# Optimization experiments

Measured on AMD Instinct MI355X. Metric: run time of the kernel, lower is better.

The kernel has to match this reference:

```python
import jax, jax.numpy as jnp
import numpy as np

B, FD, HD, G, WR = 256, 1024, 256, 64, 10.0  # batch, feature_dim, hidden_dim, grid_size, workspace_range


def _w(key, shape):
    return jax.random.normal(key, shape, dtype=jnp.float32) * 0.02


def setup_inputs() -> dict:
    key = jax.random.key(0)
    ks = jax.random.split(key, 16)
    # egocentric coordinate grid, indexing='ij', flattened to [G*G, 2]
    x = jnp.linspace(-WR / 2, WR / 2, G)
    xx, yy = jnp.meshgrid(x, x, indexing='ij')
    coords = jnp.stack([xx, yy], axis=-1).reshape(-1, 2).astype(jnp.float32)
    return {
        'features': jax.random.normal(ks[0], (B, FD), dtype=jnp.float32),
        'coords': coords,
        # context_encoder: 1024 -> 256 -> 128 -> 64
        'ce_w1': _w(ks[1], (FD, HD)), 'ce_b1': jnp.zeros((HD,), jnp.float32),
        'ce_w2': _w(ks[2], (HD, HD // 2)), 'ce_b2': jnp.zeros((HD // 2,), jnp.float32),
        'ce_w3': _w(ks[3], (HD // 2, 64)), 'ce_b3': jnp.zeros((64,), jnp.float32),
        # success_field_mlp: 66 -> 256 -> 256 -> 128 -> 1
        'sf_w1': _w(ks[4], (2 + 64, HD)), 'sf_b1': jnp.zeros((HD,), jnp.float32),
        'sf_w2': _w(ks[5], (HD, HD)), 'sf_b2': jnp.zeros((HD,), jnp.float32),
        'sf_w3': _w(ks[6], (HD, HD // 2)), 'sf_b3': jnp.zeros((HD // 2,), jnp.float32),
        'sf_w4': _w(ks[7], (HD // 2, 1)), 'sf_b4': jnp.zeros((1,), jnp.float32),
    }


def reference(features, coords, ce_w1, ce_b1, ce_w2, ce_b2, ce_w3, ce_b3,
              sf_w1, sf_b1, sf_w2, sf_b2, sf_w3, sf_b3, sf_w4, sf_b4):
    # context encoder: [B, 1024] -> [B, 64]
    z = jax.nn.relu(features @ ce_w1 + ce_b1)
    z = jax.nn.relu(z @ ce_w2 + ce_b2)
    z_c = z @ ce_w3 + ce_b3  # [B, 64]
    # first field layer split: concat([coords, z_c]) @ sf_w1 == coords@W[:2] + z_c@W[2:]
    cpart = coords @ sf_w1[:2]      # [G*G, HD]
    zpart = z_c @ sf_w1[2:]         # [B, HD]
    h = jax.nn.relu(cpart[None, :, :] + zpart[:, None, :] + sf_b1)  # [B, G*G, HD]
    h = jax.nn.relu(h @ sf_w2 + sf_b2)
    h = jax.nn.relu(h @ sf_w3 + sf_b3)
    logits = h @ sf_w4 + sf_b4      # [B, G*G, 1]
    success_fields = jax.nn.sigmoid(logits).reshape(features.shape[0], G, G)
    return success_fields
```

## Files before the change

kernel.cpp:

```cpp
#include <hip/hip_runtime.h>
#include <hip/hip_bf16.h>

typedef __bf16 bf16_t;
typedef __attribute__((ext_vector_type(4))) float f32x4;
typedef __attribute__((ext_vector_type(8))) int i32x8;

#define FD 1024
#define HD 256
#define GG 4096
#define HSTR 272

__device__ inline unsigned int pack4_fp8(float a, float b, float c, float d) {
    int v = __builtin_amdgcn_cvt_pk_fp8_f32(a, b, 0, false);
    v = __builtin_amdgcn_cvt_pk_fp8_f32(c, d, v, true);
    return (unsigned int)v;
}

#define MFMA_MX(A, B, C) \
    __builtin_amdgcn_mfma_scale_f32_16x16x128_f8f6f4((A), (B), (C), 0, 0, 0, 127, 0, 127)

__global__ __launch_bounds__(256) void prep_kernel(
    const float* __restrict__ ce_w1,
    const float* __restrict__ sf_w2,
    const float* __restrict__ sf_w3,
    float* __restrict__ w1t,
    unsigned int* __restrict__ w2t8,
    unsigned int* __restrict__ w3t8)
{
    int id = blockIdx.x * 256 + threadIdx.x;
    if (w1t != nullptr) {
        int j = id >> 10, k = id & 1023;
        w1t[id] = ce_w1[k * 256 + j];
    }
    if (id < 16384) {
        int n = id >> 6, k4 = (id & 63) << 2;
        w2t8[id] = pack4_fp8(sf_w2[(k4 + 0) * 256 + n], sf_w2[(k4 + 1) * 256 + n],
                             sf_w2[(k4 + 2) * 256 + n], sf_w2[(k4 + 3) * 256 + n]);
    }
    if (id < 8192) {
        int n = id >> 6, k4 = (id & 63) << 2;
        w3t8[id] = pack4_fp8(sf_w3[(k4 + 0) * 128 + n], sf_w3[(k4 + 1) * 128 + n],
                             sf_w3[(k4 + 2) * 128 + n], sf_w3[(k4 + 3) * 128 + n]);
    }
}

__global__ __launch_bounds__(256) void ce_kernel(
    const float* __restrict__ features,
    const float* __restrict__ ce_w1,
    const float* __restrict__ w1t,
    const float* __restrict__ ce_b1,
    const float* __restrict__ ce_w2, const float* __restrict__ ce_b2,
    const float* __restrict__ ce_w3, const float* __restrict__ ce_b3,
    const float* __restrict__ sf_w1,
    const float* __restrict__ sf_b1,
    float* __restrict__ zpart)
{
    __shared__ float fs[FD];
    __shared__ float z1[HD];
    __shared__ float z2[HD / 2];
    __shared__ float zc[64];
    const int b = blockIdx.x, t = threadIdx.x;

    #pragma unroll
    for (int i = 0; i < 4; ++i) fs[t + i * 256] = features[b * FD + t + i * 256];
    __syncthreads();

    {
        float s = ce_b1[t];
        if (w1t != nullptr) {
            const float4* wr = reinterpret_cast<const float4*>(w1t + t * FD);
            #pragma unroll 4
            for (int k = 0; k < FD / 4; ++k) {
                float4 w = wr[k];
                const float4 f = *reinterpret_cast<const float4*>(&fs[k * 4]);
                s = fmaf(w.x, f.x, s);
                s = fmaf(w.y, f.y, s);
                s = fmaf(w.z, f.z, s);
                s = fmaf(w.w, f.w, s);
            }
        } else {
            #pragma unroll 8
            for (int k = 0; k < FD; ++k) s = fmaf(fs[k], ce_w1[k * 256 + t], s);
        }
        z1[t] = s > 0.f ? s : 0.f;
    }
    __syncthreads();

    if (t < 128) {
        float s = ce_b2[t];
        #pragma unroll 8
        for (int k = 0; k < 256; ++k) s = fmaf(z1[k], ce_w2[k * 128 + t], s);
        z2[t] = s > 0.f ? s : 0.f;
    }
    __syncthreads();

    if (t < 64) {
        float s = ce_b3[t];
        #pragma unroll 8
        for (int k = 0; k < 128; ++k) s = fmaf(z2[k], ce_w3[k * 64 + t], s);
        zc[t] = s;
    }
    __syncthreads();

    {
        float s = sf_b1[t];
        #pragma unroll 8
        for (int k = 0; k < 64; ++k) s = fmaf(zc[k], sf_w1[(2 + k) * 256 + t], s);
        zpart[b * HD + t] = s;
    }
}

__global__ __launch_bounds__(512, 2) void field_kernel(
    const float* __restrict__ coords,
    const float* __restrict__ sf_w1,
    const float* __restrict__ zpart,
    const unsigned char* __restrict__ w2t8,
    const float* __restrict__ sf_b2,
    const unsigned char* __restrict__ w3t8,
    const float* __restrict__ sf_b3,
    const float* __restrict__ sf_w4,
    const float* __restrict__ sf_b4,
    float* __restrict__ out)
{
    __shared__ __attribute__((aligned(128))) unsigned char h1[4][64 * HSTR];
    __shared__ __attribute__((aligned(128))) unsigned char h2[4][64 * HSTR];
    __shared__ float partials[4][64][20];

    const int b = blockIdx.x;
    const int tid = threadIdx.x;
    const int wid = tid >> 6;
    const int lane = tid & 63;
    const int l15 = lane & 15;
    const int l4 = lane >> 4;
    const int koff = l4 * 32;

    const int cg1 = wid & 3;
    const int rg1 = wid >> 2;
    i32x8 b1f[2][4];
    #pragma unroll
    for (int ks = 0; ks < 2; ++ks)
        #pragma unroll
        for (int n = 0; n < 4; ++n)
            b1f[ks][n] = *reinterpret_cast<const i32x8*>(
                &w2t8[(cg1 * 64 + n * 16 + l15) * 256 + ks * 128 + koff]);

    const int cgrp = wid & 3, rhalf = wid >> 2;
    i32x8 w3f[2][2];
    #pragma unroll
    for (int ks = 0; ks < 2; ++ks)
        #pragma unroll
        for (int cb = 0; cb < 2; ++cb)
            w3f[ks][cb] = *reinterpret_cast<const i32x8*>(
                &w3t8[(cgrp * 32 + cb * 16 + l15) * 256 + ks * 128 + koff]);

    f32x4 b2r[4];
    #pragma unroll
    for (int n = 0; n < 4; ++n)
        b2r[n] = *reinterpret_cast<const f32x4*>(&sf_b2[cg1 * 64 + n * 16 + l4 * 4]);
    f32x4 b3r[2], w4r[2];
    #pragma unroll
    for (int cb = 0; cb < 2; ++cb) {
        b3r[cb] = *reinterpret_cast<const f32x4*>(&sf_b3[cgrp * 32 + cb * 16 + l4 * 4]);
        w4r[cb] = *reinterpret_cast<const f32x4*>(&sf_w4[cgrp * 32 + cb * 16 + l4 * 4]);
    }
    const float b4v = sf_b4[0];

    const int kc = tid & 31;
    const int rbase = tid >> 5;
    float zpf[8], waf[8], wbf[8];
    #pragma unroll
    for (int j = 0; j < 8; ++j) {
        zpf[j] = zpart[b * HD + kc * 8 + j];
        waf[j] = sf_w1[kc * 8 + j];
        wbf[j] = sf_w1[HD + kc * 8 + j];
    }
    float xvr[4];
    #pragma unroll
    for (int it = 0; it < 4; ++it)
        xvr[it] = coords[2 * (it * 16 + rbase) + 1];

    auto ld32 = [&](const unsigned char* p) -> i32x8 {
        uint4 a = *reinterpret_cast<const uint4*>(p);
        uint4 c = *reinterpret_cast<const uint4*>(p + 16);
        i32x8 r;
        r[0] = a.x; r[1] = a.y; r[2] = a.z; r[3] = a.w;
        r[4] = c.x; r[5] = c.y; r[6] = c.z; r[7] = c.w;
        return r;
    };

    auto build = [&](int t, int bi) {
        unsigned char* buf = h1[bi];
        float x0 = coords[t * 128];
        float zc8[8];
        #pragma unroll
        for (int j = 0; j < 8; ++j) zc8[j] = fmaf(x0, waf[j], zpf[j]);
        #pragma unroll
        for (int it = 0; it < 4; ++it) {
            float xv = xvr[it];
            float s[8];
            #pragma unroll
            for (int j = 0; j < 8; ++j) {
                float v = fmaf(xv, wbf[j], zc8[j]);
                s[j] = v > 0.f ? v : 0.f;
            }
            uint2 pk;
            pk.x = pack4_fp8(s[0], s[1], s[2], s[3]);
            pk.y = pack4_fp8(s[4], s[5], s[6], s[7]);
            *reinterpret_cast<uint2*>(&buf[(it * 16 + rbase) * HSTR + kc * 8]) = pk;
        }
    };

    auto subphase = [&](int t, int tm) {
        const int tg2 = t - 2;
        const bool g1 = (t < 64);
        const bool g2 = (tg2 >= 0) && (tg2 < 64);
        const unsigned char* h1c = h1[tm];
        const unsigned char* h2p = h2[(tm + 2) & 3];

        if (g1) {
            const unsigned char* r0 = h1c + (rg1 * 32 + l15) * HSTR + koff;
            const unsigned char* r1 = r0 + 16 * HSTR;
            i32x8 a00 = ld32(r0);
            i32x8 a10 = ld32(r1);
            i32x8 a01 = ld32(r0 + 128);
            i32x8 a11 = ld32(r1 + 128);

            f32x4 acc1[2][4];
            #pragma unroll
            for (int m = 0; m < 2; ++m)
                #pragma unroll
                for (int n = 0; n < 4; ++n) acc1[m][n] = b2r[n];

            __builtin_amdgcn_s_setprio(1);
            #pragma unroll
            for (int n = 0; n < 4; ++n)
                acc1[0][n] = MFMA_MX(b1f[0][n], a00, acc1[0][n]);
            #pragma unroll
            for (int n = 0; n < 4; ++n)
                acc1[1][n] = MFMA_MX(b1f[0][n], a10, acc1[1][n]);
            #pragma unroll
            for (int n = 0; n < 4; ++n)
                acc1[0][n] = MFMA_MX(b1f[1][n], a01, acc1[0][n]);
            #pragma unroll
            for (int n = 0; n < 4; ++n)
                acc1[1][n] = MFMA_MX(b1f[1][n], a11, acc1[1][n]);
            __builtin_amdgcn_s_setprio(0);

            unsigned char* h2c = h2[tm];
            #pragma unroll
            for (int n = 0; n < 4; ++n) {
                #pragma unroll
                for (int m = 0; m < 2; ++m) {
                    int row = rg1 * 32 + m * 16 + l15;
                    int col = cg1 * 64 + n * 16 + l4 * 4;
                    float x0 = fmaxf(acc1[m][n][0], 0.f);
                    float x1 = fmaxf(acc1[m][n][1], 0.f);
                    float x2 = fmaxf(acc1[m][n][2], 0.f);
                    float x3 = fmaxf(acc1[m][n][3], 0.f);
                    *reinterpret_cast<unsigned int*>(&h2c[row * HSTR + col]) =
                        pack4_fp8(x0, x1, x2, x3);
                }
            }
        }

        if (g2) {
            const unsigned char* r0 = h2p + (rhalf * 32 + l15) * HSTR + koff;
            const unsigned char* r1 = r0 + 16 * HSTR;
            i32x8 h00 = ld32(r0);
            i32x8 h10 = ld32(r1);
            i32x8 h01 = ld32(r0 + 128);
            i32x8 h11 = ld32(r1 + 128);

            f32x4 acc2[2][2] = {};
            __builtin_amdgcn_s_setprio(1);
            #pragma unroll
            for (int cb = 0; cb < 2; ++cb)
                acc2[0][cb] = MFMA_MX(w3f[0][cb], h00, acc2[0][cb]);
            #pragma unroll
            for (int cb = 0; cb < 2; ++cb)
                acc2[1][cb] = MFMA_MX(w3f[0][cb], h10, acc2[1][cb]);
            #pragma unroll
            for (int cb = 0; cb < 2; ++cb)
                acc2[0][cb] = MFMA_MX(w3f[1][cb], h01, acc2[0][cb]);
            #pragma unroll
            for (int cb = 0; cb < 2; ++cb)
                acc2[1][cb] = MFMA_MX(w3f[1][cb], h11, acc2[1][cb]);
            __builtin_amdgcn_s_setprio(0);

            #pragma unroll
            for (int rb = 0; rb < 2; ++rb) {
                float pp = 0.f;
                #pragma unroll
                for (int cb = 0; cb < 2; ++cb)
                    #pragma unroll
                    for (int i = 0; i < 4; ++i) {
                        float v = fmaxf(acc2[rb][cb][i] + b3r[cb][i], 0.f);
                        pp = fmaf(v, w4r[cb][i], pp);
                    }
                partials[(tm + 2) & 3][rhalf * 32 + rb * 16 + l15][cgrp * 4 + l4] = pp;
            }
        }

        if (t + 2 < 64) build(t + 2, (tm + 2) & 3);

        const int tf = t - 4;
        if (tf >= 0 && tid < 64) {
            const f32x4* pr = reinterpret_cast<const f32x4*>(&partials[tm][tid][0]);
            f32x4 ss = pr[0] + pr[1] + pr[2] + pr[3];
            float s = ss[0] + ss[1] + ss[2] + ss[3] + b4v;
            out[b * GG + tf * 64 + tid] = 1.f / (1.f + __expf(-s));
        }
    };

    build(0, 0);
    build(1, 1);
    __syncthreads();

    #pragma unroll 1
    for (int t0 = 0; t0 < 68; t0 += 4) {
        subphase(t0,     0);
        subphase(t0 + 1, 1);
        __syncthreads();
        subphase(t0 + 2, 2);
        subphase(t0 + 3, 3);
        __syncthreads();
    }
}

extern "C" void kernel_launch(void* const* d_in, const int* in_sizes, int n_in,
                              void* d_out, int out_size, void* d_ws, size_t ws_size,
                              hipStream_t stream)
{
    const float* features = (const float*)d_in[0];
    const float* coords   = (const float*)d_in[1];
    const float* ce_w1 = (const float*)d_in[2];
    const float* ce_b1 = (const float*)d_in[3];
    const float* ce_w2 = (const float*)d_in[4];
    const float* ce_b2 = (const float*)d_in[5];
    const float* ce_w3 = (const float*)d_in[6];
    const float* ce_b3 = (const float*)d_in[7];
    const float* sf_w1 = (const float*)d_in[8];
    const float* sf_b1 = (const float*)d_in[9];
    const float* sf_w2 = (const float*)d_in[10];
    const float* sf_b2 = (const float*)d_in[11];
    const float* sf_w3 = (const float*)d_in[12];
    const float* sf_b3 = (const float*)d_in[13];
    const float* sf_w4 = (const float*)d_in[14];
    const float* sf_b4 = (const float*)d_in[15];
    float* out = (float*)d_out;

    char* ws = (char*)d_ws;
    float*        zpart = (float*)ws;
    unsigned int* w2t8  = (unsigned int*)(ws + 262144);
    unsigned int* w3t8  = (unsigned int*)(ws + 262144 + 65536);
    float*        w1t   = (float*)(ws + 262144 + 65536 + 32768);
    const size_t need_w1t = (size_t)(262144 + 65536 + 32768) + (size_t)FD * HD * 4;
    float* w1t_ptr = (ws_size >= need_w1t) ? w1t : nullptr;

    hipLaunchKernelGGL(prep_kernel, dim3(1024), dim3(256), 0, stream,
                       ce_w1, sf_w2, sf_w3, w1t_ptr, w2t8, w3t8);
    hipLaunchKernelGGL(ce_kernel, dim3(256), dim3(256), 0, stream,
                       features, ce_w1, w1t_ptr, ce_b1, ce_w2, ce_b2, ce_w3, ce_b3,
                       sf_w1, sf_b1, zpart);
    hipLaunchKernelGGL(field_kernel, dim3(256), dim3(512), 0, stream,
                       coords, sf_w1, zpart,
                       (const unsigned char*)w2t8, sf_b2,
                       (const unsigned char*)w3t8, sf_b3, sf_w4, sf_b4, out);
}
```

Baseline: 156.5 us.

## Fuse weight prep into context encoder kernel and split-K its matvecs across 512 threads

```diff
diff --git a/kernel.cpp b/kernel.cpp
--- a/kernel.cpp
+++ b/kernel.cpp
@@ -19,95 +19,107 @@
 #define MFMA_MX(A, B, C) \
     __builtin_amdgcn_mfma_scale_f32_16x16x128_f8f6f4((A), (B), (C), 0, 0, 0, 127, 0, 127)
 
-__global__ __launch_bounds__(256) void prep_kernel(
-    const float* __restrict__ ce_w1,
-    const float* __restrict__ sf_w2,
-    const float* __restrict__ sf_w3,
-    float* __restrict__ w1t,
-    unsigned int* __restrict__ w2t8,
-    unsigned int* __restrict__ w3t8)
-{
-    int id = blockIdx.x * 256 + threadIdx.x;
-    if (w1t != nullptr) {
-        int j = id >> 10, k = id & 1023;
-        w1t[id] = ce_w1[k * 256 + j];
-    }
-    if (id < 16384) {
-        int n = id >> 6, k4 = (id & 63) << 2;
-        w2t8[id] = pack4_fp8(sf_w2[(k4 + 0) * 256 + n], sf_w2[(k4 + 1) * 256 + n],
-                             sf_w2[(k4 + 2) * 256 + n], sf_w2[(k4 + 3) * 256 + n]);
-    }
-    if (id < 8192) {
-        int n = id >> 6, k4 = (id & 63) << 2;
-        w3t8[id] = pack4_fp8(sf_w3[(k4 + 0) * 128 + n], sf_w3[(k4 + 1) * 128 + n],
-                             sf_w3[(k4 + 2) * 128 + n], sf_w3[(k4 + 3) * 128 + n]);
-    }
-}
-
-__global__ __launch_bounds__(256) void ce_kernel(
+__global__ __launch_bounds__(512) void prep_ce_kernel(
     const float* __restrict__ features,
     const float* __restrict__ ce_w1,
-    const float* __restrict__ w1t,
     const float* __restrict__ ce_b1,
     const float* __restrict__ ce_w2, const float* __restrict__ ce_b2,
     const float* __restrict__ ce_w3, const float* __restrict__ ce_b3,
     const float* __restrict__ sf_w1,
     const float* __restrict__ sf_b1,
-    float* __restrict__ zpart)
+    const float* __restrict__ sf_w2,
+    const float* __restrict__ sf_w3,
+    float* __restrict__ zpart,
+    unsigned int* __restrict__ w2t8,
+    unsigned int* __restrict__ w3t8)
 {
+    const int b = blockIdx.x;
+    const int t = threadIdx.x;
+
+    if (t < 96) {
+        int id = b * 96 + t;
+        if (id < 16384) {
+            int n = id >> 6, k4 = (id & 63) << 2;
+            w2t8[id] = pack4_fp8(sf_w2[(k4 + 0) * 256 + n], sf_w2[(k4 + 1) * 256 + n],
+                                 sf_w2[(k4 + 2) * 256 + n], sf_w2[(k4 + 3) * 256 + n]);
+        } else {
+            int id3 = id - 16384;
+            int n = id3 >> 6, k4 = (id3 & 63) << 2;
+            w3t8[id3] = pack4_fp8(sf_w3[(k4 + 0) * 128 + n], sf_w3[(k4 + 1) * 128 + n],
+                                 sf_w3[(k4 + 2) * 128 + n], sf_w3[(k4 + 3) * 128 + n]);
+        }
+    }
+
     __shared__ float fs[FD];
+    __shared__ float pp[512];
     __shared__ float z1[HD];
     __shared__ float z2[HD / 2];
     __shared__ float zc[64];
-    const int b = blockIdx.x, t = threadIdx.x;
-
-    #pragma unroll
-    for (int i = 0; i < 4; ++i) fs[t + i * 256] = features[b * FD + t + i * 256];
+
+    fs[t] = features[b * FD + t];
+    fs[t + 512] = features[b * FD + t + 512];
     __syncthreads();
 
     {
-        float s = ce_b1[t];
-        if (w1t != nullptr) {
-            const float4* wr = reinterpret_cast<const float4*>(w1t + t * FD);
-            #pragma unroll 4
-            for (int k = 0; k < FD / 4; ++k) {
-                float4 w = wr[k];
-                const float4 f = *reinterpret_cast<const float4*>(&fs[k * 4]);
-                s = fmaf(w.x, f.x, s);
-                s = fmaf(w.y, f.y, s);
-                s = fmaf(w.z, f.z, s);
-                s = fmaf(w.w, f.w, s);
-            }
-        } else {
-            #pragma unroll 8
-            for (int k = 0; k < FD; ++k) s = fmaf(fs[k], ce_w1[k * 256 + t], s);
-        }
+        const int o = t & 255, h = t >> 8;
+        float s = 0.f;
+        const float* w = ce_w1 + (h * 512) * 256 + o;
+        const float* f = fs + h * 512;
+        #pragma unroll 8
+        for (int k = 0; k < 512; ++k) s = fmaf(f[k], w[k * 256], s);
+        pp[t] = s;
+    }
+    __syncthreads();
+    if (t < 256) {
+        float s = pp[t] + pp[t + 256] + ce_b1[t];
         z1[t] = s > 0.f ? s : 0.f;
     }
     __syncthreads();
 
+    {
+        const int o = t & 127, q = t >> 7;
+        float s = 0.f;
+        const float* w = ce_w2 + (q * 64) * 128 + o;
+        const float* zz = z1 + q * 64;
+        #pragma unroll 8
+        for (int k = 0; k < 64; ++k) s = fmaf(zz[k], w[k * 128], s);
+        pp[t] = s;
+    }
+    __syncthreads();
     if (t < 128) {
-        float s = ce_b2[t];
-        #pragma unroll 8
-        for (int k = 0; k < 256; ++k) s = fmaf(z1[k], ce_w2[k * 128 + t], s);
+        float s = pp[t] + pp[t + 128] + pp[t + 256] + pp[t + 384] + ce_b2[t];
         z2[t] = s > 0.f ? s : 0.f;
     }
     __syncthreads();
 
+    {
+        const int o = t & 63, q = t >> 6;
+        float s = 0.f;
+        const float* w = ce_w3 + (q * 16) * 64 + o;
+        const float* zz = z2 + q * 16;
+        #pragma unroll
+        for (int k = 0; k < 16; ++k) s = fmaf(zz[k], w[k * 64], s);
+        pp[t] = s;
+    }
+    __syncthreads();
     if (t < 64) {
         float s = ce_b3[t];
+        #pragma unroll
+        for (int q = 0; q < 8; ++q) s += pp[t + q * 64];
+        zc[t] = s;
+    }
+    __syncthreads();
+
+    {
+        const int o = t & 255, h = t >> 8;
+        float s = 0.f;
         #pragma unroll 8
-        for (int k = 0; k < 128; ++k) s = fmaf(z2[k], ce_w3[k * 64 + t], s);
-        zc[t] = s;
-    }
-    __syncthreads();
-
-    {
-        float s = sf_b1[t];
-        #pragma unroll 8
-        for (int k = 0; k < 64; ++k) s = fmaf(zc[k], sf_w1[(2 + k) * 256 + t], s);
-        zpart[b * HD + t] = s;
-    }
+        for (int k = 0; k < 32; ++k)
+            s = fmaf(zc[h * 32 + k], sf_w1[(2 + h * 32 + k) * 256 + o], s);
+        pp[t] = s;
+    }
+    __syncthreads();
+    if (t < 256) zpart[b * HD + t] = pp[t] + pp[t + 256] + sf_b1[t];
 }
 
 __global__ __launch_bounds__(512, 2) void field_kernel(
@@ -353,15 +365,10 @@
     float*        zpart = (float*)ws;
     unsigned int* w2t8  = (unsigned int*)(ws + 262144);
     unsigned int* w3t8  = (unsigned int*)(ws + 262144 + 65536);
-    float*        w1t   = (float*)(ws + 262144 + 65536 + 32768);
-    const size_t need_w1t = (size_t)(262144 + 65536 + 32768) + (size_t)FD * HD * 4;
-    float* w1t_ptr = (ws_size >= need_w1t) ? w1t : nullptr;
-
-    hipLaunchKernelGGL(prep_kernel, dim3(1024), dim3(256), 0, stream,
-                       ce_w1, sf_w2, sf_w3, w1t_ptr, w2t8, w3t8);
-    hipLaunchKernelGGL(ce_kernel, dim3(256), dim3(256), 0, stream,
-                       features, ce_w1, w1t_ptr, ce_b1, ce_w2, ce_b2, ce_w3, ce_b3,
-                       sf_w1, sf_b1, zpart);
+
+    hipLaunchKernelGGL(prep_ce_kernel, dim3(256), dim3(512), 0, stream,
+                       features, ce_w1, ce_b1, ce_w2, ce_b2, ce_w3, ce_b3,
+                       sf_w1, sf_b1, sf_w2, sf_w3, zpart, w2t8, w3t8);
     hipLaunchKernelGGL(field_kernel, dim3(256), dim3(512), 0, stream,
                        coords, sf_w1, zpart,
                        (const unsigned char*)w2t8, sf_b2,
```

Measured after the change: 127.6 us. -18.4%, faster.
